# Performance work log

Measured on AMD Instinct MI355X. Metric: run time of the kernel, lower is better.

## Reference

```python
import jax, jax.numpy as jnp
import numpy as np

H = W = 192          # input spatial size
M = N = 96           # pooled grid (H//2, W//2)
NUM_NODES = M * N    # 9216
MAX_EDGES = 4 * NUM_NODES  # each node has at most 4 diagonal neighbors


def setup_inputs() -> dict:
    key = jax.random.key(0)
    k1, k2, k3 = jax.random.split(key, 3)
    d_coarse = jax.random.normal(k1, (1, H, W), dtype=jnp.float32)
    # torch.rand_like -> uniform [0,1); mean=0, stdev=1 in Noise module
    noise = jax.random.uniform(k2, (1, M, N), dtype=jnp.float32)
    # GraphDropout: `if self.train:` is always truthy -> dropout always applied
    dropout_mask = jax.random.bernoulli(k3, 0.5, (NUM_NODES, NUM_NODES))
    return {"d_coarse": d_coarse, "noise": noise,
            "dropout_mask": dropout_mask, "R_scale": 1}


def reference(d_coarse, noise, dropout_mask, R_scale):
    # MaxPool2d(kernel=2, stride=2) on [1, H, W]
    d_pool = d_coarse.reshape(1, M, 2, N, 2).max(axis=(2, 4))  # [1, M, N]
    # IntervalThreshold: computed on d_pool (pre-noise)
    threshold = (d_pool.max() - d_pool.min()) / min(M, N)
    # Noise: d_pool + uniform noise
    d = (d_pool + noise)[0]  # [M, N]

    # ReconGraph: `dx != 0 and dy != 0` -> ONLY diagonal neighbors.
    # labels[j, i] = count with i outer / j inner -> label(i, j) = i*N + j.
    lab = jnp.arange(NUM_NODES).reshape(M, N)
    adj = jnp.zeros((NUM_NODES, NUM_NODES), dtype=bool)
    # Two forward diagonal offsets cover all diagonal pairs; matrix is
    # symmetrized by setting both (l1, l2) and (l2, l1).
    pairs = [
        (lab[:-1, :-1], lab[1:, 1:], d[:-1, :-1], d[1:, 1:]),   # (dy,dx)=(1,1)
        (lab[:-1, 1:], lab[1:, :-1], d[:-1, 1:], d[1:, :-1]),   # (dy,dx)=(1,-1)
    ]
    for la, lb, a, b in pairs:
        conn = (jnp.abs(b - a) <= threshold).ravel()
        adj = adj.at[la.ravel(), lb.ravel()].set(conn)
        adj = adj.at[lb.ravel(), la.ravel()].set(conn)

    # GraphDropout (always active; mask is not symmetric)
    adj = adj & dropout_mask

    # convert_to_edge_index: COO indices of nonzeros, padded to static size
    rows, cols = jnp.nonzero(adj, size=MAX_EDGES, fill_value=NUM_NODES)
    return jnp.stack([rows, cols])  # [2, MAX_EDGES], sentinel = NUM_NODES
```

## Files before the change

### kernel.cpp

```cpp
#include <hip/hip_runtime.h>


#define HW 192
#define MM 96
#define NUM_NODES 9216
#define MAX_EDGES 36864
#define NB 36
#define BT 256


__global__ __launch_bounds__(BT) void k_pool(
    const float* __restrict__ dc,
    const float* __restrict__ noise,
    float* __restrict__ d_buf,
    float* __restrict__ blk_max,
    float* __restrict__ blk_min)
{
    const int t = threadIdx.x;
    const int l = blockIdx.x * BT + t;
    const int i = l / MM, j = l - i * MM;
    const float* r0 = dc + (2 * i) * HW + 2 * j;
    float2 a = *(const float2*)r0;
    float2 b = *(const float2*)(r0 + HW);
    float p = fmaxf(fmaxf(a.x, a.y), fmaxf(b.x, b.y));
    d_buf[l] = p + noise[l];

    float mx = p, mn = p;
    #pragma unroll
    for (int off = 32; off > 0; off >>= 1) {
        mx = fmaxf(mx, __shfl_down(mx, off, 64));
        mn = fminf(mn, __shfl_down(mn, off, 64));
    }
    __shared__ float smx[4], smn[4];
    const int lane = t & 63, wid = t >> 6;
    if (lane == 0) { smx[wid] = mx; smn[wid] = mn; }
    __syncthreads();
    if (t == 0) {
        blk_max[blockIdx.x] = fmaxf(fmaxf(smx[0], smx[1]), fmaxf(smx[2], smx[3]));
        blk_min[blockIdx.x] = fminf(fminf(smn[0], smn[1]), fminf(smn[2], smn[3]));
    }
}

__global__ __launch_bounds__(BT) void k_flags(
    const float* __restrict__ d_buf,
    const float* __restrict__ blk_max,
    const float* __restrict__ blk_min,
    const int*   __restrict__ mask,
    int* __restrict__ flags,
    int* __restrict__ blk_cnt)
{
    __shared__ float s_thr;
    const int t = threadIdx.x;
    if (t < 64) {
        float mx = (t < NB) ? blk_max[t] : -3.0e38f;
        float mn = (t < NB) ? blk_min[t] :  3.0e38f;
        #pragma unroll
        for (int off = 32; off > 0; off >>= 1) {
            mx = fmaxf(mx, __shfl_down(mx, off, 64));
            mn = fminf(mn, __shfl_down(mn, off, 64));
        }
        if (t == 0) s_thr = (mx - mn) / 96.0f;
    }
    __syncthreads();
    const float thr = s_thr;

    const int l = blockIdx.x * BT + t;
    const int i = l / MM, j = l - i * MM;
    const float dl = d_buf[l];
    const size_t rowbase = (size_t)l * NUM_NODES;
    int f = 0;
    if (i > 0) {
        if (j > 0      && fabsf(d_buf[l - 97] - dl) <= thr && mask[rowbase + (l - 97)]) f |= 1;
        if (j < MM - 1 && fabsf(d_buf[l - 95] - dl) <= thr && mask[rowbase + (l - 95)]) f |= 2;
    }
    if (i < MM - 1) {
        if (j > 0      && fabsf(d_buf[l + 95] - dl) <= thr && mask[rowbase + (l + 95)]) f |= 4;
        if (j < MM - 1 && fabsf(d_buf[l + 97] - dl) <= thr && mask[rowbase + (l + 97)]) f |= 8;
    }
    flags[l] = f;

    int c = __popc(f);
    #pragma unroll
    for (int off = 32; off > 0; off >>= 1) c += __shfl_down(c, off, 64);
    __shared__ int sc[4];
    const int lane = t & 63, wid = t >> 6;
    if (lane == 0) sc[wid] = c;
    __syncthreads();
    if (t == 0) blk_cnt[blockIdx.x] = sc[0] + sc[1] + sc[2] + sc[3];
}

__global__ __launch_bounds__(BT) void k_write(
    const int* __restrict__ flags,
    const int* __restrict__ blk_cnt,
    int* __restrict__ out)
{
    const int t = threadIdx.x, b = blockIdx.x;

    int blkoff = 0, total = 0;
    #pragma unroll
    for (int k = 0; k < NB; ++k) {
        int c = blk_cnt[k];
        if (k < b) blkoff += c;
        total += c;
    }

    const int l = b * BT + t;
    const int f = flags[l];
    const int c = __popc(f);

    int inc = c;
    const int lane = t & 63, wid = t >> 6;
    #pragma unroll
    for (int off = 1; off < 64; off <<= 1) {
        int v = __shfl_up(inc, off, 64);
        if (lane >= off) inc += v;
    }
    __shared__ int wtot[4];
    if (lane == 63) wtot[wid] = inc;
    __syncthreads();
    int wpre = 0;
    for (int k = 0; k < wid; ++k) wpre += wtot[k];

    int pos = blkoff + wpre + (inc - c);
    if (f & 1) { out[pos] = l; out[MAX_EDGES + pos] = l - 97; ++pos; }
    if (f & 2) { out[pos] = l; out[MAX_EDGES + pos] = l - 95; ++pos; }
    if (f & 4) { out[pos] = l; out[MAX_EDGES + pos] = l + 95; ++pos; }
    if (f & 8) { out[pos] = l; out[MAX_EDGES + pos] = l + 97; ++pos; }

    for (int idx = total + b * BT + t; idx < MAX_EDGES; idx += NUM_NODES) {
        out[idx] = NUM_NODES;
        out[MAX_EDGES + idx] = NUM_NODES;
    }
}

extern "C" void kernel_launch(void* const* d_in, const int* in_sizes, int n_in,
                              void* d_out, int out_size, void* d_ws, size_t ws_size,
                              hipStream_t stream) {
    const float* d_coarse = (const float*)d_in[0];
    const float* noise    = (const float*)d_in[1];
    const int*   mask     = (const int*)d_in[2];
    int* out = (int*)d_out;

    float* ws      = (float*)d_ws;
    float* d_buf   = ws;
    float* blk_max = ws + 9216;
    float* blk_min = ws + 9252;
    int*   flags   = (int*)(ws + 9288);
    int*   blk_cnt = (int*)(ws + 18504);

    k_pool <<<NB, BT, 0, stream>>>(d_coarse, noise, d_buf, blk_max, blk_min);
    k_flags<<<NB, BT, 0, stream>>>(d_buf, blk_max, blk_min, mask, flags, blk_cnt);
    k_write<<<NB, BT, 0, stream>>>(flags, blk_cnt, out);
}
```

Measured before the change: 377.9 us.

## Split flag computation to one thread per neighbor with ballot-based packing

The flag kernel now assigns one thread to each of a node's four diagonal neighbors, quadrupling the grid to 144 blocks. Each thread does one threshold test and one scattered mask load, and the four results are packed into the node's flag word with a wavefront ballot. This spreads the latency-bound random reads of the large mask over more threads and memory requests in flight. The write kernel now sums 144 block counts and takes its offset from the first four times its block index entries, so its serial prefix loop gets longer.

```diff
diff --git a/kernel.cpp b/kernel.cpp
--- a/kernel.cpp
+++ b/kernel.cpp
@@ -5,7 +5,8 @@
 #define MM 96
 #define NUM_NODES 9216
 #define MAX_EDGES 36864
-#define NB 36
+#define NBP 36
+#define NBF 144
 #define BT 256
 
 
@@ -52,8 +53,8 @@
     __shared__ float s_thr;
     const int t = threadIdx.x;
     if (t < 64) {
-        float mx = (t < NB) ? blk_max[t] : -3.0e38f;
-        float mn = (t < NB) ? blk_min[t] :  3.0e38f;
+        float mx = (t < NBP) ? blk_max[t] : -3.0e38f;
+        float mn = (t < NBP) ? blk_min[t] :  3.0e38f;
         #pragma unroll
         for (int off = 32; off > 0; off >>= 1) {
             mx = fmaxf(mx, __shfl_down(mx, off, 64));
@@ -64,27 +65,27 @@
     __syncthreads();
     const float thr = s_thr;
 
-    const int l = blockIdx.x * BT + t;
+    const int e = blockIdx.x * BT + t;
+    const int l = e >> 2, q = e & 3;
     const int i = l / MM, j = l - i * MM;
-    const float dl = d_buf[l];
-    const size_t rowbase = (size_t)l * NUM_NODES;
-    int f = 0;
-    if (i > 0) {
-        if (j > 0      && fabsf(d_buf[l - 97] - dl) <= thr && mask[rowbase + (l - 97)]) f |= 1;
-        if (j < MM - 1 && fabsf(d_buf[l - 95] - dl) <= thr && mask[rowbase + (l - 95)]) f |= 2;
+    const int dy = (q & 2) ? 1 : -1;
+    const int dx = (q & 1) ? 1 : -1;
+    const int nb = l + dy * MM + dx;
+    const bool ok = ((q & 2) ? (i < MM - 1) : (i > 0)) &&
+                    ((q & 1) ? (j < MM - 1) : (j > 0));
+    bool pass = false;
+    if (ok) {
+        const float diff = fabsf(d_buf[nb] - d_buf[l]);
+        if (diff <= thr)
+            pass = mask[(size_t)l * NUM_NODES + nb] != 0;
     }
-    if (i < MM - 1) {
-        if (j > 0      && fabsf(d_buf[l + 95] - dl) <= thr && mask[rowbase + (l + 95)]) f |= 4;
-        if (j < MM - 1 && fabsf(d_buf[l + 97] - dl) <= thr && mask[rowbase + (l + 97)]) f |= 8;
-    }
-    flags[l] = f;
+    const unsigned long long bal = __ballot(pass);
+    const int lane = t & 63, wid = t >> 6;
+    if ((lane & 3) == 0)
+        flags[l] = (int)((bal >> (lane & 60)) & 0xFull);
 
-    int c = __popc(f);
-    #pragma unroll
-    for (int off = 32; off > 0; off >>= 1) c += __shfl_down(c, off, 64);
     __shared__ int sc[4];
-    const int lane = t & 63, wid = t >> 6;
-    if (lane == 0) sc[wid] = c;
+    if (lane == 0) sc[wid] = __popcll(bal);
     __syncthreads();
     if (t == 0) blk_cnt[blockIdx.x] = sc[0] + sc[1] + sc[2] + sc[3];
 }
@@ -97,10 +98,10 @@
     const int t = threadIdx.x, b = blockIdx.x;
 
     int blkoff = 0, total = 0;
-    #pragma unroll
-    for (int k = 0; k < NB; ++k) {
+    #pragma unroll 8
+    for (int k = 0; k < NBF; ++k) {
         int c = blk_cnt[k];
-        if (k < b) blkoff += c;
+        if (k < 4 * b) blkoff += c;
         total += c;
     }
 
@@ -148,7 +149,7 @@
     int*   flags   = (int*)(ws + 9288);
     int*   blk_cnt = (int*)(ws + 18504);
 
-    k_pool <<<NB, BT, 0, stream>>>(d_coarse, noise, d_buf, blk_max, blk_min);
-    k_flags<<<NB, BT, 0, stream>>>(d_buf, blk_max, blk_min, mask, flags, blk_cnt);
-    k_write<<<NB, BT, 0, stream>>>(flags, blk_cnt, out);
+    k_pool <<<NBP, BT, 0, stream>>>(d_coarse, noise, d_buf, blk_max, blk_min);
+    k_flags<<<NBF, BT, 0, stream>>>(d_buf, blk_max, blk_min, mask, flags, blk_cnt);
+    k_write<<<NBP, BT, 0, stream>>>(flags, blk_cnt, out);
 }
```

Result: no change. 377.0 us (-0.3%).
